# Kernel tuning notes

Measured on AMD Instinct MI355X. Metric: run time of the kernel, lower is better.

The kernel has to match this reference:

```python
import jax, jax.numpy as jnp
import numpy as np

NEG_BIG = -10000000000.0  # value used by masked_fill_ in the original


def setup_inputs() -> dict:
    S, B, H = 2048, 16, 1024
    key = jax.random.key(0)
    ks = jax.random.split(key, 6)
    return {
        "hidden": jax.random.normal(ks[0], (1, B, H), dtype=jnp.float32),
        "hidden_sequence": jax.random.normal(ks[1], (S, B, H), dtype=jnp.float32),
        "input_masks": jax.random.randint(ks[2], (S, B), 0, 2) > 0,
        "W_att": jax.random.normal(ks[3], (H, 2 * H), dtype=jnp.float32) * (1.0 / np.sqrt(2 * H)),
        "b_att": jax.random.normal(ks[4], (H,), dtype=jnp.float32) * 0.01,
        "v": jax.random.normal(ks[5], (H,), dtype=jnp.float32),
    }


def reference(hidden, hidden_sequence, input_masks, W_att, b_att, v):
    S, B, H = hidden_sequence.shape
    # concat score: tanh(Linear([hidden; hidden_seq])) . v  -> [S, B]
    h = jnp.broadcast_to(hidden, (S, B, H))
    concat_hidden = jnp.concatenate([h, hidden_sequence], axis=2)  # [S, B, 2H]
    energy = jnp.tanh(jnp.einsum('sbk,hk->sbh', concat_hidden, W_att) + b_att)
    score = jnp.einsum('sbh,h->sb', energy, v)  # [S, B]
    # masked_fill_(~mask, -1e10); the original's .permute(1,0) result is discarded
    score = jnp.where(input_masks, score, jnp.float32(NEG_BIG))
    # faithful: softmax over dim=1 of the [S, B] energy (as in the source)
    attention_weight = jax.nn.softmax(score, axis=1)  # [S, B]
    # bmm([B,1,S], [B,S,H]) -> [B,1,H] -> permute(1,0,2) -> [1,B,H]
    context = jnp.einsum('sb,sbh->bh', attention_weight, hidden_sequence)[None, :, :]
    return context
```

## Files before the change

### kernel.cpp

```cpp
#include <hip/hip_runtime.h>
#include <math.h>

#define S_LEN 2048
#define B_SZ  16
#define H_SZ  1024
#define M_SZ  32768

typedef __attribute__((ext_vector_type(8))) _Float16 half8;
typedef __attribute__((ext_vector_type(4))) float f32x4;

__device__ __forceinline__ unsigned pack2h(float a, float b) {
    _Float16 ha = (_Float16)a, hb = (_Float16)b;
    unsigned short ua = __builtin_bit_cast(unsigned short, ha);
    unsigned short ub = __builtin_bit_cast(unsigned short, hb);
    return (unsigned)ua | ((unsigned)ub << 16);
}

__device__ __forceinline__ int phys_off(int r, int sl) {
    return ((r >> 1) << 7) + ((((r & 1) << 2 | sl) ^ ((r >> 1) & 7)) << 4);
}

__device__ __forceinline__ void dma16(const void* g, void* l) {
    __builtin_amdgcn_global_load_lds(
        (const __attribute__((address_space(1))) unsigned int*)g,
        (__attribute__((address_space(3))) unsigned int*)l, 16, 0, 0);
}

__global__ void k_hidden_part(const float* __restrict__ hidden,
                              const float* __restrict__ W,
                              const float* __restrict__ b_att,
                              float* __restrict__ hp) {
    int gid  = blockIdx.x * blockDim.x + threadIdx.x;
    int wave = gid >> 6;
    int lane = threadIdx.x & 63;
    int b = wave >> 10;
    int h = wave & 1023;
    const float* x = hidden + b * H_SZ;
    const float* w = W + (size_t)h * (2 * H_SZ);
    float acc = 0.f;
    #pragma unroll
    for (int k = 0; k < H_SZ; k += 64) acc += x[k + lane] * w[k + lane];
    #pragma unroll
    for (int off = 32; off; off >>= 1) acc += __shfl_down(acc, off, 64);
    if (lane == 0) hp[b * H_SZ + h] = acc + b_att[h];
}

__global__ void k_conv_tiles(const float* __restrict__ src,
                             unsigned short* __restrict__ dst,
                             int rowStride, int colOff) {
    int t = blockIdx.x * 256 + threadIdx.x;
    int sl = t & 3, r = (t >> 2) & 127, kt = (t >> 9) & 31, p = t >> 14;
    const float* s = src + (size_t)(p * 128 + r) * rowStride + colOff + kt * 32 + sl * 8;
    float4 f0 = *(const float4*)s;
    float4 f1 = *(const float4*)(s + 4);
    uint4 u;
    u.x = pack2h(f0.x, f0.y); u.y = pack2h(f0.z, f0.w);
    u.z = pack2h(f1.x, f1.y); u.w = pack2h(f1.z, f1.w);
    *(uint4*)((char*)dst + (size_t)(p * 32 + kt) * 8192 + phys_off(r, sl)) = u;
}

#define SA2   0
#define SB2   8192
#define SBUF2 16384

__global__ __launch_bounds__(256, 4)
void k_score_dma2(const unsigned short* __restrict__ Xsw,
                  const unsigned short* __restrict__ Wsw,
                  const float* __restrict__ hp,
                  const float* __restrict__ v,
                  float* __restrict__ score_part) {
    __shared__ char lds[2 * SBUF2];

    const int t = threadIdx.x;
    int wg = (blockIdx.x & 7) * 256 + (blockIdx.x >> 3);
    const int mp = wg >> 3;
    const int m0 = mp * 128;
    const int nt = wg & 7;
    const int n0 = nt * 128;

    const int lane = t & 63, wid = t >> 6;
    const int wm = wid >> 1, wn = wid & 1;
    const int lr = lane & 15, lq = lane >> 4;

    const char* At = (const char*)Xsw + (size_t)mp * 32 * 8192 + wid * 1024 + lane * 16;
    const char* Bt = (const char*)Wsw + (size_t)nt * 32 * 8192 + wid * 1024 + lane * 16;

    int aro[4], bro[4];
    #pragma unroll
    for (int i = 0; i < 4; ++i) {
        aro[i] = phys_off(wm * 64 + i * 16 + lr, lq);
        bro[i] = phys_off(wn * 64 + i * 16 + lr, lq);
    }

    f32x4 acc[4][4];
    #pragma unroll
    for (int i = 0; i < 4; ++i)
        #pragma unroll
        for (int j = 0; j < 4; ++j) acc[i][j] = (f32x4)0.f;

#define DMA2(bufbase, kt)                                                      \
    {                                                                          \
        const char* a = At + (size_t)(kt) * 8192;                              \
        const char* b = Bt + (size_t)(kt) * 8192;                              \
        dma16(a,        (bufbase) + SA2 + wid * 1024);                         \
        dma16(a + 4096, (bufbase) + SA2 + 4096 + wid * 1024);                  \
        dma16(b,        (bufbase) + SB2 + wid * 1024);                         \
        dma16(b + 4096, (bufbase) + SB2 + 4096 + wid * 1024);                  \
    }

    DMA2(lds, 0);
    __syncthreads();

    for (int kt = 0; kt < 32; ++kt) {
        char* cur = lds + (kt & 1) * SBUF2;
        char* nxt = lds + ((kt & 1) ^ 1) * SBUF2;
        if (kt < 31) DMA2(nxt, kt + 1);

        half8 ah[4], bh[4];
        #pragma unroll
        for (int i = 0; i < 4; ++i) ah[i] = *(const half8*)(cur + SA2 + aro[i]);
        #pragma unroll
        for (int j = 0; j < 4; ++j) bh[j] = *(const half8*)(cur + SB2 + bro[j]);

        #pragma unroll
        for (int i = 0; i < 4; ++i)
            #pragma unroll
            for (int j = 0; j < 4; ++j)
                acc[i][j] = __builtin_amdgcn_mfma_f32_16x16x32_f16(ah[i], bh[j], acc[i][j], 0, 0, 0);

        __syncthreads();
    }

    float* red = (float*)lds;
    #pragma unroll
    for (int i = 0; i < 4; ++i) {
        #pragma unroll
        for (int r = 0; r < 4; ++r) {
            const int b = lq * 4 + r;
            float s = 0.f;
            #pragma unroll
            for (int j = 0; j < 4; ++j) {
                const int c = n0 + wn * 64 + j * 16 + lr;
                s += v[c] * tanhf(acc[i][j][r] + hp[b * H_SZ + c]);
            }
            s += __shfl_xor(s, 1);
            s += __shfl_xor(s, 2);
            s += __shfl_xor(s, 4);
            s += __shfl_xor(s, 8);
            if (lr == 0)
                red[wn * 128 + wm * 64 + i * 16 + lq * 4 + r] = s;
        }
    }
    __syncthreads();
    if (t < 128)
        score_part[nt * M_SZ + m0 + t] = red[t] + red[128 + t];
#undef DMA2
}

__global__ __launch_bounds__(256, 3)
void k_score_dma(const float* __restrict__ X,
                 const unsigned short* __restrict__ Wsw,
                 const float* __restrict__ hp,
                 const float* __restrict__ v,
                 float* __restrict__ score_part) {
    __shared__ char lds[2 * SBUF2];

    const int t = threadIdx.x;
    int wg = (blockIdx.x & 7) * 256 + (blockIdx.x >> 3);
    const int m0 = (wg >> 3) * 128;
    const int nt = wg & 7;
    const int n0 = nt * 128;

    const int lane = t & 63, wid = t >> 6;
    const int wm = wid >> 1, wn = wid & 1;
    const int lr = lane & 15, lq = lane >> 4;

    const int srow = t >> 1, shalf = t & 1;
    const float* Xp = X + (size_t)(m0 + srow) * 1024 + shalf * 16;
    const int aOff0 = phys_off(srow, shalf * 2 + 0);
    const int aOff1 = phys_off(srow, shalf * 2 + 1);

    const unsigned short* Bp = Wsw + (size_t)(nt * 32) * 4096 + wid * 512 + lane * 8;

    int aro[4], bro[4];
    #pragma unroll
    for (int i = 0; i < 4; ++i) {
        aro[i] = phys_off(wm * 64 + i * 16 + lr, lq);
        bro[i] = phys_off(wn * 64 + i * 16 + lr, lq);
    }

    f32x4 acc[4][4];
    #pragma unroll
    for (int i = 0; i < 4; ++i)
        #pragma unroll
        for (int j = 0; j < 4; ++j) acc[i][j] = (f32x4)0.f;

    float4 ax[4];

#define LOADA(kt)                                                              \
    {                                                                          \
        const float* p = Xp + (kt) * 32;                                       \
        ax[0] = *(const float4*)(p);                                           \
        ax[1] = *(const float4*)(p + 4);                                       \
        ax[2] = *(const float4*)(p + 8);                                       \
        ax[3] = *(const float4*)(p + 12);                                      \
    }

#define DMAB(bufbase, kt)                                                      \
    {                                                                          \
        const unsigned short* s0 = Bp + (size_t)(kt) * 4096;                   \
        dma16(s0,        (bufbase) + SB2 + wid * 1024);                        \
        dma16(s0 + 2048, (bufbase) + SB2 + wid * 1024 + 4096);                 \
    }

#define STAGEA(bufbase)                                                        \
    {                                                                          \
        uint4 p0, p1;                                                          \
        p0.x = pack2h(ax[0].x, ax[0].y); p0.y = pack2h(ax[0].z, ax[0].w);      \
        p0.z = pack2h(ax[1].x, ax[1].y); p0.w = pack2h(ax[1].z, ax[1].w);      \
        p1.x = pack2h(ax[2].x, ax[2].y); p1.y = pack2h(ax[2].z, ax[2].w);      \
        p1.z = pack2h(ax[3].x, ax[3].y); p1.w = pack2h(ax[3].z, ax[3].w);      \
        *(uint4*)((bufbase) + SA2 + aOff0) = p0;                               \
        *(uint4*)((bufbase) + SA2 + aOff1) = p1;                               \
    }

    LOADA(0);
    DMAB(lds, 0);
    STAGEA(lds);
    __syncthreads();

    for (int kt = 0; kt < 32; ++kt) {
        char* cur = lds + (kt & 1) * SBUF2;
        char* nxt = lds + ((kt & 1) ^ 1) * SBUF2;
        if (kt < 31) {
            LOADA(kt + 1);
            DMAB(nxt, kt + 1);
        }

        half8 ah[4], bh[4];
        #pragma unroll
        for (int i = 0; i < 4; ++i) ah[i] = *(const half8*)(cur + SA2 + aro[i]);
        #pragma unroll
        for (int j = 0; j < 4; ++j) bh[j] = *(const half8*)(cur + SB2 + bro[j]);

        #pragma unroll
        for (int i = 0; i < 4; ++i)
            #pragma unroll
            for (int j = 0; j < 4; ++j)
                acc[i][j] = __builtin_amdgcn_mfma_f32_16x16x32_f16(ah[i], bh[j], acc[i][j], 0, 0, 0);

        if (kt < 31) STAGEA(nxt);
        __syncthreads();
    }

    float* red = (float*)lds;
    #pragma unroll
    for (int i = 0; i < 4; ++i) {
        #pragma unroll
        for (int r = 0; r < 4; ++r) {
            const int b = lq * 4 + r;
            float s = 0.f;
            #pragma unroll
            for (int j = 0; j < 4; ++j) {
                const int c = n0 + wn * 64 + j * 16 + lr;
                s += v[c] * tanhf(acc[i][j][r] + hp[b * H_SZ + c]);
            }
            s += __shfl_xor(s, 1);
            s += __shfl_xor(s, 2);
            s += __shfl_xor(s, 4);
            s += __shfl_xor(s, 8);
            if (lr == 0)
                red[wn * 128 + wm * 64 + i * 16 + lq * 4 + r] = s;
        }
    }
    __syncthreads();
    if (t < 128)
        score_part[nt * M_SZ + m0 + t] = red[t] + red[128 + t];
#undef LOADA
#undef DMAB
#undef STAGEA
}

__global__ void k_softmax(const float* __restrict__ part,
                          const int* __restrict__ masks,
                          float* __restrict__ wts) {
    int s = blockIdx.x * blockDim.x + threadIdx.x;
    if (s >= S_LEN) return;
    float vals[16];
    float mx = -INFINITY;
    #pragma unroll
    for (int b = 0; b < 16; ++b) {
        int m = s * 16 + b;
        float sc = 0.f;
        #pragma unroll
        for (int p = 0; p < 8; ++p) sc += part[p * M_SZ + m];
        sc = masks[m] ? sc : -1e10f;
        vals[b] = sc;
        mx = fmaxf(mx, sc);
    }
    float sum = 0.f;
    #pragma unroll
    for (int b = 0; b < 16; ++b) { vals[b] = __expf(vals[b] - mx); sum += vals[b]; }
    float inv = 1.f / sum;
    #pragma unroll
    for (int b = 0; b < 16; ++b) wts[s * 16 + b] = vals[b] * inv;
}

__global__ void k_context_partial(const float* __restrict__ wts,
                                  const float* __restrict__ X,
                                  float* __restrict__ partial) {
    int b = blockIdx.x & 15;
    int c = blockIdx.x >> 4;
    int h = threadIdx.x * 4;
    float4 acc = make_float4(0.f, 0.f, 0.f, 0.f);
    for (int s = c * 128; s < c * 128 + 128; ++s) {
        float w = wts[s * 16 + b];
        float4 x = *(const float4*)(X + (size_t)(s * 16 + b) * 1024 + h);
        acc.x += w * x.x; acc.y += w * x.y; acc.z += w * x.z; acc.w += w * x.w;
    }
    *(float4*)(partial + (size_t)(c * 16 + b) * 1024 + h) = acc;
}

__global__ void k_context_reduce(const float* __restrict__ partial,
                                 float* __restrict__ out) {
    int o = blockIdx.x * blockDim.x + threadIdx.x;
    int b = o >> 10, h = o & 1023;
    float s = 0.f;
    #pragma unroll
    for (int cc = 0; cc < 16; ++cc) s += partial[(size_t)(cc * 16 + b) * 1024 + h];
    out[o] = s;
}

extern "C" void kernel_launch(void* const* d_in, const int* in_sizes, int n_in,
                              void* d_out, int out_size, void* d_ws, size_t ws_size,
                              hipStream_t stream) {
    const float* hidden = (const float*)d_in[0];
    const float* hseq   = (const float*)d_in[1];
    const int*   masks  = (const int*)d_in[2];
    const float* W      = (const float*)d_in[3];
    const float* b_att  = (const float*)d_in[4];
    const float* v      = (const float*)d_in[5];
    float* out = (float*)d_out;

    float* wsf        = (float*)d_ws;
    float* hp         = wsf;
    float* wts        = wsf + 16384;
    float* score_part = wts + 32768;
    float* partial    = score_part + 8 * M_SZ;
    unsigned short* Wsw = (unsigned short*)(partial + 262144);
    unsigned short* Xsw = (unsigned short*)((char*)Wsw + 2 * 1024 * 1024);
    const size_t WS_FAST = (size_t)(16384 + 32768 + 262144 + 262144) * 4
                         + 2ull * 1024 * 1024 + 64ull * 1024 * 1024;

    hipLaunchKernelGGL(k_hidden_part, dim3(4096), dim3(256), 0, stream, hidden, W, b_att, hp);
    hipLaunchKernelGGL(k_conv_tiles,  dim3(512),  dim3(256), 0, stream, W, Wsw, 2048, 1024);
    if (ws_size >= WS_FAST) {
        hipLaunchKernelGGL(k_conv_tiles,  dim3(16384), dim3(256), 0, stream, hseq, Xsw, 1024, 0);
        hipLaunchKernelGGL(k_score_dma2,  dim3(2048),  dim3(256), 0, stream, Xsw, Wsw, hp, v, score_part);
    } else {
        hipLaunchKernelGGL(k_score_dma,   dim3(2048),  dim3(256), 0, stream, hseq, Wsw, hp, v, score_part);
    }
    hipLaunchKernelGGL(k_softmax,         dim3(8),   dim3(256), 0, stream, score_part, masks, wts);
    hipLaunchKernelGGL(k_context_partial, dim3(256), dim3(256), 0, stream, wts, hseq, partial);
    hipLaunchKernelGGL(k_context_reduce,  dim3(64),  dim3(256), 0, stream, partial, out);
}
```

Measured before the change: 359.1 us.

## Triple-buffer score GEMM, fast tanh, transpose partials, f16 context from swizzled X

The score GEMM moves from double to triple-buffered DMA prefetch, using explicit vmcnt waits, one barrier per k-step and raised priority around the MFMAs. tanhf is replaced by an exp/rcp approximation. Score partials are stored row-major so softmax can read them with float4 loads. Context is now computed from the fp16 swizzled copy of hidden_sequence, split into 32 chunks, which halves the bytes read in that stage but adds fp16 rounding to the weighted sum. Occupancy hint drops from 4 to 3 blocks per SM because of the larger LDS footprint.

```diff
diff --git a/kernel.cpp b/kernel.cpp
--- a/kernel.cpp
+++ b/kernel.cpp
@@ -7,6 +7,7 @@
 #define M_SZ  32768
 
 typedef __attribute__((ext_vector_type(8))) _Float16 half8;
+typedef __attribute__((ext_vector_type(4))) _Float16 half4;
 typedef __attribute__((ext_vector_type(4))) float f32x4;
 
 __device__ __forceinline__ unsigned pack2h(float a, float b) {
@@ -14,6 +15,11 @@
     unsigned short ua = __builtin_bit_cast(unsigned short, ha);
     unsigned short ub = __builtin_bit_cast(unsigned short, hb);
     return (unsigned)ua | ((unsigned)ub << 16);
+}
+
+__device__ __forceinline__ float tanh_fast(float x) {
+    float e = __expf(2.f * x);
+    return __builtin_fmaf(-2.f, __builtin_amdgcn_rcpf(e + 1.f), 1.f);
 }
 
 __device__ __forceinline__ int phys_off(int r, int sl) {
@@ -63,13 +69,13 @@
 #define SB2   8192
 #define SBUF2 16384
 
-__global__ __launch_bounds__(256, 4)
-void k_score_dma2(const unsigned short* __restrict__ Xsw,
+__global__ __launch_bounds__(256, 3)
+void k_score_pipe(const unsigned short* __restrict__ Xsw,
                   const unsigned short* __restrict__ Wsw,
                   const float* __restrict__ hp,
                   const float* __restrict__ v,
                   float* __restrict__ score_part) {
-    __shared__ char lds[2 * SBUF2];
+    __shared__ char lds[3 * SBUF2];
 
     const int t = threadIdx.x;
     int wg = (blockIdx.x & 7) * 256 + (blockIdx.x >> 3);
@@ -108,28 +114,36 @@
         dma16(b + 4096, (bufbase) + SB2 + 4096 + wid * 1024);                  \
     }
 
-    DMA2(lds, 0);
-    __syncthreads();
+    char* cb0 = lds;
+    char* cb1 = lds + SBUF2;
+    char* cb2 = lds + 2 * SBUF2;
+    DMA2(cb0, 0);
+    DMA2(cb1, 1);
 
     for (int kt = 0; kt < 32; ++kt) {
-        char* cur = lds + (kt & 1) * SBUF2;
-        char* nxt = lds + ((kt & 1) ^ 1) * SBUF2;
-        if (kt < 31) DMA2(nxt, kt + 1);
+        if (kt < 31) { asm volatile("s_waitcnt vmcnt(4)" ::: "memory"); }
+        else         { asm volatile("s_waitcnt vmcnt(0)" ::: "memory"); }
+        __builtin_amdgcn_s_barrier();
+        __builtin_amdgcn_sched_barrier(0);
+        if (kt < 30) DMA2(cb2, kt + 2);
 
         half8 ah[4], bh[4];
         #pragma unroll
-        for (int i = 0; i < 4; ++i) ah[i] = *(const half8*)(cur + SA2 + aro[i]);
-        #pragma unroll
-        for (int j = 0; j < 4; ++j) bh[j] = *(const half8*)(cur + SB2 + bro[j]);
-
+        for (int i = 0; i < 4; ++i) ah[i] = *(const half8*)(cb0 + SA2 + aro[i]);
+        #pragma unroll
+        for (int j = 0; j < 4; ++j) bh[j] = *(const half8*)(cb0 + SB2 + bro[j]);
+
+        __builtin_amdgcn_s_setprio(1);
         #pragma unroll
         for (int i = 0; i < 4; ++i)
             #pragma unroll
             for (int j = 0; j < 4; ++j)
                 acc[i][j] = __builtin_amdgcn_mfma_f32_16x16x32_f16(ah[i], bh[j], acc[i][j], 0, 0, 0);
-
-        __syncthreads();
-    }
+        __builtin_amdgcn_s_setprio(0);
+
+        char* tmp = cb0; cb0 = cb1; cb1 = cb2; cb2 = tmp;
+    }
+    __syncthreads();
 
     float* red = (float*)lds;
     #pragma unroll
@@ -141,7 +155,7 @@
             #pragma unroll
             for (int j = 0; j < 4; ++j) {
                 const int c = n0 + wn * 64 + j * 16 + lr;
-                s += v[c] * tanhf(acc[i][j][r] + hp[b * H_SZ + c]);
+                s += v[c] * tanh_fast(acc[i][j][r] + hp[b * H_SZ + c]);
             }
             s += __shfl_xor(s, 1);
             s += __shfl_xor(s, 2);
@@ -153,7 +167,7 @@
     }
     __syncthreads();
     if (t < 128)
-        score_part[nt * M_SZ + m0 + t] = red[t] + red[128 + t];
+        score_part[(size_t)(m0 + t) * 8 + nt] = red[t] + red[128 + t];
 #undef DMA2
 }
 
@@ -263,7 +277,7 @@
             #pragma unroll
             for (int j = 0; j < 4; ++j) {
                 const int c = n0 + wn * 64 + j * 16 + lr;
-                s += v[c] * tanhf(acc[i][j][r] + hp[b * H_SZ + c]);
+                s += v[c] * tanh_fast(acc[i][j][r] + hp[b * H_SZ + c]);
             }
             s += __shfl_xor(s, 1);
             s += __shfl_xor(s, 2);
@@ -275,26 +289,25 @@
     }
     __syncthreads();
     if (t < 128)
-        score_part[nt * M_SZ + m0 + t] = red[t] + red[128 + t];
+        score_part[(size_t)(m0 + t) * 8 + nt] = red[t] + red[128 + t];
 #undef LOADA
 #undef DMAB
 #undef STAGEA
 }
 
-__global__ void k_softmax(const float* __restrict__ part,
+__global__ void k_softmax(const float* __restrict__ sp,
                           const int* __restrict__ masks,
                           float* __restrict__ wts) {
     int s = blockIdx.x * blockDim.x + threadIdx.x;
     if (s >= S_LEN) return;
+    const float4* base = (const float4*)(sp + (size_t)s * 128);
     float vals[16];
     float mx = -INFINITY;
     #pragma unroll
     for (int b = 0; b < 16; ++b) {
-        int m = s * 16 + b;
-        float sc = 0.f;
-        #pragma unroll
-        for (int p = 0; p < 8; ++p) sc += part[p * M_SZ + m];
-        sc = masks[m] ? sc : -1e10f;
+        float4 p0 = base[b * 2], p1 = base[b * 2 + 1];
+        float sc = ((p0.x + p0.y) + (p0.z + p0.w)) + ((p1.x + p1.y) + (p1.z + p1.w));
+        sc = masks[s * 16 + b] ? sc : -1e10f;
         vals[b] = sc;
         mx = fmaxf(mx, sc);
     }
@@ -304,6 +317,40 @@
     float inv = 1.f / sum;
     #pragma unroll
     for (int b = 0; b < 16; ++b) wts[s * 16 + b] = vals[b] * inv;
+}
+
+__global__ __launch_bounds__(256)
+void k_context_f16(const float* __restrict__ wts,
+                   const unsigned short* __restrict__ Xsw,
+                   float* __restrict__ partial) {
+    const int t = threadIdx.x;
+    const int b = blockIdx.x & 15;
+    const int c = blockIdx.x >> 4;
+    const int kt = t >> 3;
+    const int sl = (t >> 1) & 3;
+    const int e8 = (t & 1) * 8;
+
+    int po[8];
+    #pragma unroll
+    for (int j = 0; j < 8; ++j) po[j] = phys_off(b + j * 16, sl) + e8;
+
+    const char* base = (const char*)Xsw + ((size_t)(c * 8) * 32 + kt) * 8192;
+    float4 acc = make_float4(0.f, 0.f, 0.f, 0.f);
+    #pragma unroll
+    for (int o = 0; o < 8; ++o) {
+        const char* tb = base + (size_t)o * 32 * 8192;
+        #pragma unroll
+        for (int j = 0; j < 8; ++j) {
+            const int s = c * 64 + o * 8 + j;
+            float w = wts[s * 16 + b];
+            half4 x = *(const half4*)(tb + po[j]);
+            acc.x += w * (float)x[0];
+            acc.y += w * (float)x[1];
+            acc.z += w * (float)x[2];
+            acc.w += w * (float)x[3];
+        }
+    }
+    *(float4*)(partial + (size_t)(c * 16 + b) * 1024 + t * 4) = acc;
 }
 
 __global__ void k_context_partial(const float* __restrict__ wts,
@@ -313,7 +360,7 @@
     int c = blockIdx.x >> 4;
     int h = threadIdx.x * 4;
     float4 acc = make_float4(0.f, 0.f, 0.f, 0.f);
-    for (int s = c * 128; s < c * 128 + 128; ++s) {
+    for (int s = c * 64; s < c * 64 + 64; ++s) {
         float w = wts[s * 16 + b];
         float4 x = *(const float4*)(X + (size_t)(s * 16 + b) * 1024 + h);
         acc.x += w * x.x; acc.y += w * x.y; acc.z += w * x.z; acc.w += w * x.w;
@@ -327,7 +374,7 @@
     int b = o >> 10, h = o & 1023;
     float s = 0.f;
     #pragma unroll
-    for (int cc = 0; cc < 16; ++cc) s += partial[(size_t)(cc * 16 + b) * 1024 + h];
+    for (int cc = 0; cc < 32; ++cc) s += partial[(size_t)(cc * 16 + b) * 1024 + h];
     out[o] = s;
 }
 
@@ -347,20 +394,22 @@
     float* wts        = wsf + 16384;
     float* score_part = wts + 32768;
     float* partial    = score_part + 8 * M_SZ;
-    unsigned short* Wsw = (unsigned short*)(partial + 262144);
+    unsigned short* Wsw = (unsigned short*)(partial + 32 * 16 * 1024);
     unsigned short* Xsw = (unsigned short*)((char*)Wsw + 2 * 1024 * 1024);
-    const size_t WS_FAST = (size_t)(16384 + 32768 + 262144 + 262144) * 4
+    const size_t WS_FAST = (size_t)(16384 + 32768 + 262144 + 524288) * 4
                          + 2ull * 1024 * 1024 + 64ull * 1024 * 1024;
 
     hipLaunchKernelGGL(k_hidden_part, dim3(4096), dim3(256), 0, stream, hidden, W, b_att, hp);
     hipLaunchKernelGGL(k_conv_tiles,  dim3(512),  dim3(256), 0, stream, W, Wsw, 2048, 1024);
     if (ws_size >= WS_FAST) {
-        hipLaunchKernelGGL(k_conv_tiles,  dim3(16384), dim3(256), 0, stream, hseq, Xsw, 1024, 0);
-        hipLaunchKernelGGL(k_score_dma2,  dim3(2048),  dim3(256), 0, stream, Xsw, Wsw, hp, v, score_part);
+        hipLaunchKernelGGL(k_conv_tiles,   dim3(16384), dim3(256), 0, stream, hseq, Xsw, 1024, 0);
+        hipLaunchKernelGGL(k_score_pipe,   dim3(2048),  dim3(256), 0, stream, Xsw, Wsw, hp, v, score_part);
+        hipLaunchKernelGGL(k_softmax,      dim3(8),     dim3(256), 0, stream, score_part, masks, wts);
+        hipLaunchKernelGGL(k_context_f16,  dim3(512),   dim3(256), 0, stream, wts, Xsw, partial);
     } else {
-        hipLaunchKernelGGL(k_score_dma,   dim3(2048),  dim3(256), 0, stream, hseq, Wsw, hp, v, score_part);
-    }
-    hipLaunchKernelGGL(k_softmax,         dim3(8),   dim3(256), 0, stream, score_part, masks, wts);
-    hipLaunchKernelGGL(k_context_partial, dim3(256), dim3(256), 0, stream, wts, hseq, partial);
-    hipLaunchKernelGGL(k_context_reduce,  dim3(64),  dim3(256), 0, stream, partial, out);
-}
+        hipLaunchKernelGGL(k_score_dma,    dim3(2048),  dim3(256), 0, stream, hseq, Wsw, hp, v, score_part);
+        hipLaunchKernelGGL(k_softmax,      dim3(8),     dim3(256), 0, stream, score_part, masks, wts);
+        hipLaunchKernelGGL(k_context_partial, dim3(512), dim3(256), 0, stream, wts, hseq, partial);
+    }
+    hipLaunchKernelGGL(k_context_reduce, dim3(64), dim3(256), 0, stream, partial, out);
+}
```

Result: faster. 334.1 us (-7.0%).
